# Optimization experiments

Hardware: AMD Instinct MI355X
Metric: run time of the kernel (lower is better)

The kernel has to match this reference:

```python
import jax, jax.numpy as jnp
import numpy as np

EPS = 1e-5
AVG_D = 32.0


def setup_inputs() -> dict:
    key = jax.random.key(0)
    ks = jax.random.split(key, 12)
    Ns, Nd, E, D, K = 1_000_000, 100_000, 3_200_000, 16, 2
    Fs, Fd, V = 4, 4, 100_000
    F = Fd + K  # predictor fields
    inp = {}
    inp["Cat_src"] = jax.random.randint(ks[0], (Ns, Fs), 0, V)
    inp["Cat_dst"] = jax.random.randint(ks[1], (Nd, Fd), 0, V)
    inp["src_ids"] = jax.random.randint(ks[2], (E,), 0, Ns)
    inp["dst_ids"] = jax.random.randint(ks[3], (E,), 0, Nd)
    inp["label"] = jax.random.randint(ks[4], (Nd,), 0, 2)
    inp["w"] = jax.random.normal(ks[5], (V, D), dtype=jnp.float32) * 0.05
    inp["W_agg"] = jax.random.normal(ks[6], (K, 12 * D, D), dtype=jnp.float32) * 0.05
    inp["b_agg"] = jnp.zeros((K, D), jnp.float32)
    inp["w_lin"] = jax.random.normal(ks[7], (F * D,), dtype=jnp.float32) * 0.05
    inp["b_lin"] = jnp.zeros((1,), jnp.float32)
    inp["W1"] = jax.random.normal(ks[8], (F * D, 64), dtype=jnp.float32) * 0.05
    inp["b1"] = jnp.zeros((64,), jnp.float32)
    inp["W2"] = jax.random.normal(ks[9], (64, 32), dtype=jnp.float32) * 0.05
    inp["b2"] = jnp.zeros((32,), jnp.float32)
    inp["W3"] = jax.random.normal(ks[10], (32, 1), dtype=jnp.float32) * 0.05
    inp["b3"] = jnp.zeros((1,), jnp.float32)
    return inp


def reference(Cat_src, Cat_dst, src_ids, dst_ids, label, w, W_agg, b_agg,
              w_lin, b_lin, W1, b1, W2, b2, W3, b3):
    Nd = Cat_dst.shape[0]
    # --- node embedding: gather cat fields, RowEmb with modes [mean, max] -> [Ns, K, D]
    emb = w[Cat_src]                                      # [Ns, Fs, D]
    h_src = jnp.stack([emb.mean(1), emb.max(1)], axis=1)  # [Ns, K, D]
    # --- multi-aggregator message passing (copy_u + segment min/max/mean, std via mean of h^2)
    m = h_src[src_ids]                                    # [E, K, D]
    deg = jax.ops.segment_sum(jnp.ones(src_ids.shape, m.dtype), dst_ids, Nd)
    safe = jnp.maximum(deg, 1.0)[:, None, None]
    mean = jax.ops.segment_sum(m, dst_ids, Nd) / safe
    mean2 = jax.ops.segment_sum(m * m, dst_ids, Nd) / safe
    has = (deg > 0)[:, None, None]
    mn = jnp.where(has, jax.ops.segment_min(m, dst_ids, Nd), 0.0)
    mx = jnp.where(has, jax.ops.segment_max(m, dst_ids, Nd), 0.0)
    std = jnp.sqrt(jax.nn.relu(mean2 - mean * mean) + EPS)
    tmp = jnp.concatenate([mean, mn, mx, std], axis=-1)   # [Nd, K, 4D]
    # --- PNA degree scalers: identity / amplification / attenuation
    logd = jnp.log(deg + 1.0)
    log_avg = jnp.log(AVG_D + 1.0)
    amp = (logd / log_avg)[:, None, None]
    att = jnp.where(logd > 0, log_avg / jnp.maximum(logd, EPS), 0.0)[:, None, None]
    scaled = jnp.concatenate([tmp, tmp * amp, tmp * att], axis=-1)  # [Nd, K, 12D]
    mes = jnp.einsum('nkf,kfd->nkd', scaled, W_agg) + b_agg          # [Nd, K, D]
    # --- final block: concat dst cat embeddings with aggregated messages
    x = jnp.concatenate([w[Cat_dst], mes], axis=1)        # [Nd, F, D]
    # --- DeepFM predictor: linear + FM pairwise + deep MLP
    flat = x.reshape(Nd, -1)
    lin = flat @ w_lin + b_lin[0]
    s = x.sum(1)
    fm = 0.5 * ((s * s) - (x * x).sum(1)).sum(-1)
    h = jax.nn.relu(flat @ W1 + b1)
    h = jax.nn.relu(h @ W2 + b2)
    deep = (h @ W3 + b3)[:, 0]
    pred = jax.nn.sigmoid(lin + fm + deep)
    return (pred, label)
```

## Files before the change

kernel.cpp:

```cpp
#include <hip/hip_runtime.h>
#include <math.h>

#define EPSF 1e-5f
#define BSH  5
#define BSZ  32
#define MAXB 4096
#define SBH  9
#define MAXSB 256
#define TILE 4096
#define SEG  8
#define BCAP 1472
#define XPAD 100
#define X2PADS 72
#define HISTB 512
#define NPACK 14336

typedef __attribute__((ext_vector_type(8))) short short8;
typedef __attribute__((ext_vector_type(4))) float float4v;

__device__ inline unsigned f2bf_rne(float x) {
    unsigned u = __float_as_uint(x);
    u += 0x7FFF + ((u >> 16) & 1);
    return u >> 16;
}
__device__ inline short bf16_of(float x) { return (short)f2bf_rne(x); }
__device__ inline float bf2f_lo(unsigned hv) { return __uint_as_float(hv << 16); }
__device__ inline float bf2f_hi(unsigned hv) { return __uint_as_float(hv & 0xFFFF0000u); }
__device__ inline float bf2f_s(ushort s) { return __uint_as_float((unsigned)s << 16); }

__global__ void cast_w(const float* __restrict__ w, ushort* __restrict__ wb, int n) {
    int i4 = (blockIdx.x * 256 + threadIdx.x) * 4;
    if (i4 + 3 < n) {
        float4 v = *(const float4*)(w + i4);
        ushort4 o;
        o.x = (ushort)f2bf_rne(v.x); o.y = (ushort)f2bf_rne(v.y);
        o.z = (ushort)f2bf_rne(v.z); o.w = (ushort)f2bf_rne(v.w);
        *(ushort4*)(wb + i4) = o;
    } else {
        for (int j = i4; j < n; ++j) wb[j] = (ushort)f2bf_rne(w[j]);
    }
}

__global__ __launch_bounds__(256) void zero_pack(
    int* bcount, int nb,
    const float* __restrict__ W_agg, const float* __restrict__ W1,
    const float* __restrict__ W2, ushort* __restrict__ wpack)
{
    int nzb = (nb + 255) >> 8;
    if ((int)blockIdx.x < nzb) {
        int i = blockIdx.x * 256 + threadIdx.x;
        if (i < nb) bcount[i] = 0;
        return;
    }
    for (int it = threadIdx.x; it < 1792; it += 256) {
        if (it < 768) {
            int t_g = it >> 6; int rem = it & 63;
            int q = rem >> 4, col = rem & 15;
            int kvar = t_g / 6, t = t_g % 6;
            const float* src = W_agg + kvar * 3072 + (t * 32 + q * 8) * 16 + col;
            ushort* dst = wpack + (size_t)it * 8;
#pragma unroll
            for (int j = 0; j < 8; ++j) dst[j] = (ushort)f2bf_rne(src[j * 16]);
        } else if (it < 1536) {
            int i2 = it - 768;
            int t = i2 >> 8; int rem = i2 & 255;
            int q = rem >> 6, col = rem & 63;
            const float* src = W1 + (t * 32 + q * 8) * 64 + col;
            ushort* dst = wpack + 6144 + (size_t)i2 * 8;
#pragma unroll
            for (int j = 0; j < 8; ++j) dst[j] = (ushort)f2bf_rne(src[j * 64]);
        } else {
            int i2 = it - 1536;
            int t = i2 >> 7; int rem = i2 & 127;
            int q = rem >> 5, col = rem & 31;
            const float* src = W2 + (t * 32 + q * 8) * 32 + col;
            ushort* dst = wpack + 12288 + (size_t)i2 * 8;
#pragma unroll
            for (int j = 0; j < 8; ++j) dst[j] = (ushort)f2bf_rne(src[j * 32]);
        }
    }
}

__global__ __launch_bounds__(256) void build_h_hist(
    const int* __restrict__ Cat_src, const ushort* __restrict__ wb,
    unsigned* __restrict__ h, int Ns,
    const int* __restrict__ dst_ids, int* bcount, int E, int nb)
{
    __shared__ int hsh[MAXB];
    if (blockIdx.x < HISTB) {
        for (int i = threadIdx.x; i < nb; i += 256) hsh[i] = 0;
        __syncthreads();
        int stride = HISTB * 256;
        for (int e = blockIdx.x * 256 + threadIdx.x; e < E; e += stride)
            atomicAdd(&hsh[dst_ids[e] >> BSH], 1);
        __syncthreads();
        for (int i = threadIdx.x; i < nb; i += 256) {
            int c = hsh[i];
            if (c) atomicAdd(&bcount[i], c);
        }
        return;
    }
    int gid = (blockIdx.x - HISTB) * 256 + threadIdx.x;
    int s = gid >> 4;
    if (s >= Ns) return;
    int lane = threadIdx.x & 63;
    int d = lane & 15;
    int c = Cat_src[s * 4 + (d & 3)];
    float vs = 0.f, vm = -INFINITY;
#pragma unroll
    for (int f = 0; f < 4; ++f) {
        int id = __shfl(c, (lane & 48) + f, 64);
        float a = bf2f_s(wb[id * 16 + d]);
        vs += a; vm = fmaxf(vm, a);
    }
    unsigned packed = f2bf_rne(vs * 0.25f) | (f2bf_rne(vm) << 16);
    __builtin_nontemporal_store(packed, &h[s * 16 + d]);
}

__global__ __launch_bounds__(256) void scan_buckets(const int* __restrict__ bcount,
                                                    int* bstart, int* sbcursor,
                                                    int* gcur, int nb) {
    __shared__ int lsum[256];
    int tid = threadIdx.x;
    int v[16];
    int s = 0;
#pragma unroll
    for (int j = 0; j < 16; ++j) {
        int idx = tid * 16 + j;
        v[j] = (idx < nb) ? bcount[idx] : 0;
        s += v[j];
    }
    lsum[tid] = s;
    __syncthreads();
    for (int off = 1; off < 256; off <<= 1) {
        int y = (tid >= off) ? lsum[tid - off] : 0;
        __syncthreads();
        lsum[tid] += y;
        __syncthreads();
    }
    int run = lsum[tid] - s;
    if (tid * 16 < nb) sbcursor[tid] = run;
#pragma unroll
    for (int j = 0; j < 16; ++j) {
        int idx = tid * 16 + j;
        if (idx < nb) { bstart[idx] = run; gcur[idx] = run; }
        run += v[j];
    }
}

__global__ __launch_bounds__(256) void scatter_sb(
    const int* __restrict__ src_ids, const int* __restrict__ dst_ids,
    int* sbcursor, unsigned* __restrict__ pairs1, int E, int nsb)
{
    __shared__ int cnt[MAXSB];
    __shared__ int base[MAXSB];
    int tid = threadIdx.x;
    int t0 = blockIdx.x * TILE;
    for (int i = tid; i < nsb; i += 256) cnt[i] = 0;
    __syncthreads();
    int rank[TILE / 256];
#pragma unroll
    for (int j = 0; j < TILE / 256; ++j) {
        int e = t0 + j * 256 + tid;
        rank[j] = (e < E) ? atomicAdd(&cnt[dst_ids[e] >> SBH], 1) : 0;
    }
    __syncthreads();
    for (int i = tid; i < nsb; i += 256) {
        int c = cnt[i];
        base[i] = c ? atomicAdd(&sbcursor[i], c) : 0;
    }
    __syncthreads();
#pragma unroll
    for (int j = 0; j < TILE / 256; ++j) {
        int e = t0 + j * 256 + tid;
        if (e < E) {
            int d = dst_ids[e];
            int sb = d >> SBH;
            pairs1[base[sb] + rank[j]] =
                ((unsigned)src_ids[e] << 9) | (unsigned)(d & 511);
        }
    }
}

__global__ __launch_bounds__(256) void scatter_fine(
    const unsigned* __restrict__ pairs1, const int* __restrict__ bstart,
    int* gcur, unsigned* __restrict__ pairs2, int nb, int nsb, int E)
{
    __shared__ int cnt[16];
    __shared__ int base[16];
    int S = blockIdx.x >> 3, seg = blockIdx.x & (SEG - 1);
    int tid = threadIdx.x;
    int sbs = bstart[S << 4];
    int sbe = (S == nsb - 1) ? E : bstart[(S + 1) << 4];
    int len = sbe - sbs;
    int per = (len + SEG - 1) / SEG;
    int s0 = sbs + seg * per;
    int s1 = s0 + per; if (s1 > sbe) s1 = sbe;
    if (tid < 16) cnt[tid] = 0;
    __syncthreads();
    int rank[12];
    unsigned pv[12];
    int nit = (s1 - s0 + 255) >> 8;
    if (nit > 12) nit = 12;
    for (int j = 0; j < nit; ++j) {
        int e = s0 + j * 256 + tid;
        if (e < s1) {
            unsigned p = __builtin_nontemporal_load(&pairs1[e]);
            pv[j] = p;
            rank[j] = atomicAdd(&cnt[(p >> 5) & 15], 1);
        }
    }
    __syncthreads();
    if (tid < 16) {
        int idx = (S << 4) + tid;
        int c = cnt[tid];
        base[tid] = (c && idx < nb) ? atomicAdd(&gcur[idx], c) : 0;
    }
    __syncthreads();
    for (int j = 0; j < nit; ++j) {
        int e = s0 + j * 256 + tid;
        if (e < s1) {
            unsigned p = pv[j];
            pairs2[base[(p >> 5) & 15] + rank[j]] = p;
        }
    }
}


__device__ inline void bucket_sort(const unsigned* __restrict__ pairs,
                                   int gbase, int cnt,
                                   unsigned* sp, int* hist, int* ofs, int* start,
                                   int tid)
{
    if (tid < BSZ) hist[tid] = 0;
    __syncthreads();
    for (int i = tid; i < cnt; i += 256)
        atomicAdd(&hist[__builtin_nontemporal_load(&pairs[gbase + i]) & (BSZ - 1)], 1);
    __syncthreads();
    if (tid < BSZ) ofs[tid] = hist[tid];
    __syncthreads();
    for (int off = 1; off < BSZ; off <<= 1) {
        int y = (tid < BSZ && tid >= off) ? ofs[tid - off] : 0;
        __syncthreads();
        if (tid < BSZ) ofs[tid] += y;
        __syncthreads();
    }
    if (tid < BSZ) {
        start[tid] = ofs[tid] - hist[tid];
        ofs[tid] = ofs[tid] - hist[tid];
    }
    __syncthreads();
    for (int i = tid; i < cnt; i += 256) {
        unsigned p = __builtin_nontemporal_load(&pairs[gbase + i]);
        int r = atomicAdd(&ofs[p & (BSZ - 1)], 1);
        sp[r] = p;
    }
    __syncthreads();
}

__device__ inline void emit_stats(float sum0, float sq0, float mn0, float mx0,
                                  float sum1, float sq1, float mn1, float mx1,
                                  int dg, int n, int lane, int sub,
                                  ushort* __restrict__ tmpb, int* __restrict__ deg_out)
{
#pragma unroll
    for (int off = 16; off <= 32; off <<= 1) {
        sum0 += __shfl_xor(sum0, off); sq0 += __shfl_xor(sq0, off);
        mn0 = fminf(mn0, __shfl_xor(mn0, off)); mx0 = fmaxf(mx0, __shfl_xor(mx0, off));
        sum1 += __shfl_xor(sum1, off); sq1 += __shfl_xor(sq1, off);
        mn1 = fminf(mn1, __shfl_xor(mn1, off)); mx1 = fmaxf(mx1, __shfl_xor(mx1, off));
    }
    float safe = fmaxf((float)dg, 1.f);
    float r = 1.f / safe;
    bool has = dg > 0;
    float mean0 = sum0 * r, mean1 = sum1 * r;
    float sd0 = sqrtf(fmaxf(sq0 * r - mean0 * mean0, 0.f) + EPSF);
    float sd1 = sqrtf(fmaxf(sq1 * r - mean1 * mean1, 0.f) + EPSF);
    float v0 = (sub == 0) ? mean0 : (sub == 1) ? (has ? mn0 : 0.f)
             : (sub == 2) ? (has ? mx0 : 0.f) : sd0;
    float v1 = (sub == 0) ? mean1 : (sub == 1) ? (has ? mn1 : 0.f)
             : (sub == 2) ? (has ? mx1 : 0.f) : sd1;
    ushort* tp = tmpb + (size_t)n * 128;
    tp[lane] = (ushort)f2bf_rne(v0);
    tp[64 + lane] = (ushort)f2bf_rne(v1);
    if (lane == 0) deg_out[n] = dg;
}

__global__ __launch_bounds__(256) void agg_from_h(
    const unsigned* __restrict__ h,
    const int* __restrict__ bstart, const int* __restrict__ bcount,
    const unsigned* __restrict__ pairs,
    ushort* __restrict__ tmpb, int* __restrict__ deg_out, int Nd)
{
    __shared__ unsigned sp[BCAP];
    __shared__ int hist[BSZ];
    __shared__ int ofs[BSZ];
    __shared__ int start[BSZ];
    int b = blockIdx.x, tid = threadIdx.x;
    int cnt = bcount[b];
    int gbase = bstart[b];
    if (cnt > BCAP) cnt = BCAP;
    bucket_sort(pairs, gbase, cnt, sp, hist, ofs, start, tid);

    int wv = tid >> 6, lane = tid & 63, sub = lane >> 4, d = lane & 15;
#pragma unroll 1
    for (int q = 0; q < 8; ++q) {
        int dl = wv * 8 + q;
        int n = b * BSZ + dl;
        if (n >= Nd) break;
        int st = start[dl], dg = hist[dl];
        float sum0 = 0.f, sq0 = 0.f, mn0 = INFINITY, mx0 = -INFINITY;
        float sum1 = 0.f, sq1 = 0.f, mn1 = INFINITY, mx1 = -INFINITY;
        int nt = (dg + 15) >> 4;
        for (int t = 0; t < nt; ++t) {
            int base = t * 16 + sub;
            unsigned hv[4];
#pragma unroll
            for (int j = 0; j < 4; ++j) {
                int e = base + j * 4;
                int ec = (e < dg) ? e : (dg - 1);
                unsigned p = sp[st + ec];
                hv[j] = h[(p >> 9) * 16 + d];
            }
#pragma unroll
            for (int j = 0; j < 4; ++j) {
                int e = base + j * 4;
                if (e < dg) {
                    float me = bf2f_lo(hv[j]);
                    float vm = bf2f_hi(hv[j]);
                    sum0 += me; sq0 += me * me;
                    mn0 = fminf(mn0, me); mx0 = fmaxf(mx0, me);
                    sum1 += vm; sq1 += vm * vm;
                    mn1 = fminf(mn1, vm); mx1 = fmaxf(mx1, vm);
                }
            }
        }
        emit_stats(sum0, sq0, mn0, mx0, sum1, sq1, mn1, mx1,
                   dg, n, lane, sub, tmpb, deg_out);
    }
}

__global__ __launch_bounds__(256) void agg_from_w(
    const int* __restrict__ Cat_src, const float* __restrict__ w,
    const ushort* __restrict__ wb, int use_bf,
    const int* __restrict__ bstart, const int* __restrict__ bcount,
    const unsigned* __restrict__ pairs,
    ushort* __restrict__ tmpb, int* __restrict__ deg_out, int Nd)
{
    __shared__ unsigned sp[BCAP];
    __shared__ int hist[BSZ];
    __shared__ int ofs[BSZ];
    __shared__ int start[BSZ];
    int b = blockIdx.x, tid = threadIdx.x;
    int cnt = bcount[b];
    int gbase = bstart[b];
    if (cnt > BCAP) cnt = BCAP;
    bucket_sort(pairs, gbase, cnt, sp, hist, ofs, start, tid);

    int wv = tid >> 6, lane = tid & 63, sub = lane >> 4, d = lane & 15;
#pragma unroll 1
    for (int q = 0; q < 8; ++q) {
        int dl = wv * 8 + q;
        int n = b * BSZ + dl;
        if (n >= Nd) break;
        int st = start[dl], dg = hist[dl];
        float sum0 = 0.f, sq0 = 0.f, mn0 = INFINITY, mx0 = -INFINITY;
        float sum1 = 0.f, sq1 = 0.f, mn1 = INFINITY, mx1 = -INFINITY;
        int nt = (dg + 3) >> 2;
        for (int t = 0; t < nt; ++t) {
            int e4 = t * 4 + sub;
            int ec = (e4 < dg) ? e4 : (dg - 1);
            unsigned p = sp[st + ec];
            int src = (int)(p >> 9);
            int cat = Cat_src[src * 4 + (d & 3)];
            float vs = 0.f, vm = -INFINITY;
            if (use_bf) {
#pragma unroll
                for (int f = 0; f < 4; ++f) {
                    int id = __shfl(cat, sub * 16 + f, 64);
                    float a = bf2f_s(wb[id * 16 + d]);
                    vs += a; vm = fmaxf(vm, a);
                }
            } else {
#pragma unroll
                for (int f = 0; f < 4; ++f) {
                    int id = __shfl(cat, sub * 16 + f, 64);
                    float a = w[id * 16 + d];
                    vs += a; vm = fmaxf(vm, a);
                }
            }
            if (e4 < dg) {
                float me = vs * 0.25f;
                sum0 += me; sq0 += me * me;
                mn0 = fminf(mn0, me); mx0 = fmaxf(mx0, me);
                sum1 += vm; sq1 += vm * vm;
                mn1 = fminf(mn1, vm); mx1 = fmaxf(mx1, vm);
            }
        }
        emit_stats(sum0, sq0, mn0, mx0, sum1, sq1, mn1, mx1,
                   dg, n, lane, sub, tmpb, deg_out);
    }
}

__global__ __launch_bounds__(256) void finalize_mfma(
    const int* __restrict__ Cat_dst, const int* __restrict__ label,
    const float* __restrict__ w, const ushort* __restrict__ wpack,
    const float* __restrict__ b_agg,
    const float* __restrict__ w_lin, const float* __restrict__ b_lin,
    const float* __restrict__ b1, const float* __restrict__ b2,
    const float* __restrict__ W3, const float* __restrict__ b3,
    const int* __restrict__ deg_arr, const ushort* __restrict__ tmpb,
    float* __restrict__ out, int Nd)
{
    __shared__ __align__(16) float sx[4][16 * XPAD];
    __shared__ __align__(16) ushort sx2[4][16 * X2PADS];
    __shared__ float sdeep[4][16];

    int tid = threadIdx.x;
    int wv = tid >> 6, lane = tid & 63;
    int q = lane >> 4, m = lane & 15;
    int n0 = (blockIdx.x * 4 + wv) * 16;
    int n = n0 + m;
    int nc = (n < Nd) ? n : (Nd - 1);

    float* X = sx[wv];
    ushort* X2 = sx2[wv];

    float fdeg = (float)deg_arr[nc];
    float logd = logf(fdeg + 1.f);
    const float logavg = logf(33.0f);
    float amp = logd / logavg;
    float att = (logd > 0.f) ? (logavg / fmaxf(logd, EPSF)) : 0.f;
    float ampr[4], attr[4];
#pragma unroll
    for (int r = 0; r < 4; ++r) {
        ampr[r] = __shfl(amp, q * 4 + r, 64);
        attr[r] = __shfl(att, q * 4 + r, 64);
    }

    const ushort* tpn = tmpb + (size_t)nc * 128;
#pragma unroll
    for (int kvar = 0; kvar < 2; ++kvar) {
        short8 af0 = *(const short8*)(tpn + kvar * 64 + q * 8);
        short8 af1 = *(const short8*)(tpn + kvar * 64 + 32 + q * 8);
        float4v aI = {0.f,0.f,0.f,0.f}, aA = {0.f,0.f,0.f,0.f}, aT = {0.f,0.f,0.f,0.f};
#pragma unroll
        for (int sb = 0; sb < 3; ++sb) {
            short8 b0 = *(const short8*)(wpack +
                (size_t)(((kvar * 6 + sb * 2) * 4 + q) * 16 + m) * 8);
            short8 b1v = *(const short8*)(wpack +
                (size_t)(((kvar * 6 + sb * 2 + 1) * 4 + q) * 16 + m) * 8);
            if (sb == 0) {
                aI = __builtin_amdgcn_mfma_f32_16x16x32_bf16(af0, b0, aI, 0, 0, 0);
                aI = __builtin_amdgcn_mfma_f32_16x16x32_bf16(af1, b1v, aI, 0, 0, 0);
            } else if (sb == 1) {
                aA = __builtin_amdgcn_mfma_f32_16x16x32_bf16(af0, b0, aA, 0, 0, 0);
                aA = __builtin_amdgcn_mfma_f32_16x16x32_bf16(af1, b1v, aA, 0, 0, 0);
            } else {
                aT = __builtin_amdgcn_mfma_f32_16x16x32_bf16(af0, b0, aT, 0, 0, 0);
                aT = __builtin_amdgcn_mfma_f32_16x16x32_bf16(af1, b1v, aT, 0, 0, 0);
            }
        }
        float bias = b_agg[kvar * 16 + m];
#pragma unroll
        for (int r = 0; r < 4; ++r)
            X[(q * 4 + r) * XPAD + 64 + kvar * 16 + m] =
                aI[r] + ampr[r] * aA[r] + attr[r] * aT[r] + bias;
    }
    {
        int nl = lane >> 2, fl = lane & 3;
        int nn = n0 + nl;
        int nnc = (nn < Nd) ? nn : (Nd - 1);
        int cid = Cat_dst[nnc * 4 + fl];
        const float4* R = (const float4*)(w + (size_t)cid * 16);
        float* xp = X + nl * XPAD + fl * 16;
        *(float4*)(xp + 0)  = R[0];
        *(float4*)(xp + 4)  = R[1];
        *(float4*)(xp + 8)  = R[2];
        *(float4*)(xp + 12) = R[3];
    }
    __syncthreads();

    float lin = 0.f, sq = 0.f;
    float sd[16];
#pragma unroll
    for (int u = 0; u < 16; ++u) sd[u] = 0.f;
    {
        const float* xp = X + m * XPAD + q * 16;
        const float* wl = w_lin + q * 16;
#pragma unroll
        for (int u = 0; u < 16; ++u) {
            float v = xp[u];
            lin += v * wl[u]; sq += v * v; sd[u] += v;
        }
    }
    if (q < 2) {
        const float* xp = X + m * XPAD + (4 + q) * 16;
        const float* wl = w_lin + (4 + q) * 16;
#pragma unroll
        for (int u = 0; u < 16; ++u) {
            float v = xp[u];
            lin += v * wl[u]; sq += v * v; sd[u] += v;
        }
    }
#pragma unroll
    for (int off = 16; off <= 32; off <<= 1) {
        lin += __shfl_xor(lin, off);
        sq  += __shfl_xor(sq, off);
#pragma unroll
        for (int u = 0; u < 16; ++u) sd[u] += __shfl_xor(sd[u], off);
    }
    float fm = 0.f;
#pragma unroll
    for (int u = 0; u < 16; ++u) fm += sd[u] * sd[u];
    fm = 0.5f * (fm - sq);

    short8 xa[3];
#pragma unroll
    for (int t = 0; t < 3; ++t) {
        const float* xp = X + m * XPAD + t * 32 + q * 8;
        float4 a0 = *(const float4*)xp;
        float4 a1 = *(const float4*)(xp + 4);
        xa[t][0] = bf16_of(a0.x); xa[t][1] = bf16_of(a0.y);
        xa[t][2] = bf16_of(a0.z); xa[t][3] = bf16_of(a0.w);
        xa[t][4] = bf16_of(a1.x); xa[t][5] = bf16_of(a1.y);
        xa[t][6] = bf16_of(a1.z); xa[t][7] = bf16_of(a1.w);
    }
#pragma unroll
    for (int nt = 0; nt < 4; ++nt) {
        float4v acc = {0.f, 0.f, 0.f, 0.f};
#pragma unroll
        for (int t = 0; t < 3; ++t) {
            short8 bf = *(const short8*)(wpack + 6144 +
                (size_t)((t * 4 + q) * 64 + nt * 16 + m) * 8);
            acc = __builtin_amdgcn_mfma_f32_16x16x32_bf16(xa[t], bf, acc, 0, 0, 0);
        }
        float bb = b1[nt * 16 + m];
#pragma unroll
        for (int r = 0; r < 4; ++r)
            X2[(q * 4 + r) * X2PADS + nt * 16 + m] =
                (ushort)f2bf_rne(fmaxf(acc[r] + bb, 0.f));
    }
    __syncthreads();

    short8 ha[2];
#pragma unroll
    for (int t = 0; t < 2; ++t)
        ha[t] = *(const short8*)(X2 + m * X2PADS + t * 32 + q * 8);
    float dp[4] = {0.f, 0.f, 0.f, 0.f};
#pragma unroll
    for (int nt = 0; nt < 2; ++nt) {
        float4v acc = {0.f, 0.f, 0.f, 0.f};
#pragma unroll
        for (int t = 0; t < 2; ++t) {
            short8 bf = *(const short8*)(wpack + 12288 +
                (size_t)((t * 4 + q) * 32 + nt * 16 + m) * 8);
            acc = __builtin_amdgcn_mfma_f32_16x16x32_bf16(ha[t], bf, acc, 0, 0, 0);
        }
        float bb = b2[nt * 16 + m];
        float w3 = W3[nt * 16 + m];
#pragma unroll
        for (int r = 0; r < 4; ++r)
            dp[r] += fmaxf(acc[r] + bb, 0.f) * w3;
    }
#pragma unroll
    for (int off = 1; off <= 8; off <<= 1) {
#pragma unroll
        for (int r = 0; r < 4; ++r) dp[r] += __shfl_xor(dp[r], off);
    }
    if (m < 4)
        sdeep[wv][q * 4 + m] = (m == 0) ? dp[0] : (m == 1) ? dp[1]
                             : (m == 2) ? dp[2] : dp[3];
    __syncthreads();
    float deep = sdeep[wv][m];

    if (q == 0 && n < Nd) {
        float z = lin + b_lin[0] + fm + deep + b3[0];
        float pred = 1.f / (1.f + expf(-z));
        out[n] = pred;
        out[Nd + n] = (float)label[n];
    }
}

extern "C" void kernel_launch(void* const* d_in, const int* in_sizes, int n_in,
                              void* d_out, int out_size, void* d_ws, size_t ws_size,
                              hipStream_t stream) {
    const int*   Cat_src = (const int*)d_in[0];
    const int*   Cat_dst = (const int*)d_in[1];
    const int*   src_ids = (const int*)d_in[2];
    const int*   dst_ids = (const int*)d_in[3];
    const int*   label   = (const int*)d_in[4];
    const float* w       = (const float*)d_in[5];
    const float* W_agg   = (const float*)d_in[6];
    const float* b_agg   = (const float*)d_in[7];
    const float* w_lin   = (const float*)d_in[8];
    const float* b_lin   = (const float*)d_in[9];
    const float* W1      = (const float*)d_in[10];
    const float* b1      = (const float*)d_in[11];
    const float* W2      = (const float*)d_in[12];
    const float* b2      = (const float*)d_in[13];
    const float* W3      = (const float*)d_in[14];
    const float* b3      = (const float*)d_in[15];

    int E  = in_sizes[2];
    int Nd = in_sizes[4];
    int Ns = in_sizes[0] / 4;
    int VD = in_sizes[5];
    int nb  = (Nd + BSZ - 1) >> BSH;
    int nsb = (nb + 15) >> 4;

    int* bcount   = (int*)d_ws;
    int* bstart   = bcount + MAXB;
    int* sbcursor = bstart + MAXB;
    int* gcur     = sbcursor + MAXSB;
    int* deg      = gcur + MAXB;
    unsigned* pairs1 = (unsigned*)(deg + Nd);
    unsigned* pairs2 = pairs1 + E;
    size_t off_tmp = (((size_t)(MAXB * 3 + MAXSB + Nd) + 2 * (size_t)E) * 4 + 255)
                     & ~(size_t)255;
    ushort* tmpb = (ushort*)((char*)d_ws + off_tmp);
    ushort* wpack = tmpb + (size_t)Nd * 128;
    ushort* w_bf16 = wpack + NPACK;
    unsigned* h  = (unsigned*)(w_bf16 + VD);

    size_t need_common = off_tmp + (size_t)Nd * 256 + (size_t)NPACK * 2;
    size_t need_A = need_common + (size_t)VD * 2;
    size_t need_B = need_A + (size_t)Ns * 64;
    int mode = (ws_size >= need_B) ? 2 : (ws_size >= need_A) ? 1 : 0;

    float* out = (float*)d_out;

    int nzb = (nb + 255) >> 8;
    hipLaunchKernelGGL(zero_pack, dim3(nzb + 1), dim3(256), 0, stream,
                       bcount, nb, W_agg, W1, W2, wpack);
    if (mode >= 1)
        hipLaunchKernelGGL(cast_w, dim3((VD / 4 + 255) / 256), dim3(256),
                           0, stream, w, w_bf16, VD);
    if (mode == 2) {
        int hb = (int)(((size_t)Ns * 16 + 255) / 256);
        hipLaunchKernelGGL(build_h_hist, dim3(HISTB + hb), dim3(256), 0, stream,
                           Cat_src, w_bf16, h, Ns, dst_ids, bcount, E, nb);
    } else {
        hipLaunchKernelGGL(build_h_hist, dim3(HISTB), dim3(256), 0, stream,
                           Cat_src, w_bf16, h, 0, dst_ids, bcount, E, nb);
    }
    hipLaunchKernelGGL(scan_buckets, dim3(1), dim3(256), 0, stream,
                       bcount, bstart, sbcursor, gcur, nb);
    hipLaunchKernelGGL(scatter_sb, dim3((E + TILE - 1) / TILE), dim3(256), 0, stream,
                       src_ids, dst_ids, sbcursor, pairs1, E, nsb);
    hipLaunchKernelGGL(scatter_fine, dim3(nsb * SEG), dim3(256), 0, stream,
                       pairs1, bstart, gcur, pairs2, nb, nsb, E);
    if (mode == 2) {
        hipLaunchKernelGGL(agg_from_h, dim3(nb), dim3(256), 0, stream,
                           h, bstart, bcount, pairs2, tmpb, deg, Nd);
    } else {
        hipLaunchKernelGGL(agg_from_w, dim3(nb), dim3(256), 0, stream,
                           Cat_src, w, w_bf16, mode, bstart, bcount, pairs2,
                           tmpb, deg, Nd);
    }
    hipLaunchKernelGGL(finalize_mfma, dim3((Nd + 63) / 64), dim3(256), 0, stream,
                       Cat_dst, label, w, wpack, b_agg, w_lin, b_lin,
                       b1, b2, W3, b3, deg, tmpb, out, Nd);
}
```

Measured before the change: 322.0 us.

## Regroup setup kernels, co-schedule h build with scatter, widen gather unroll, bf16 X tile

Merges zero_pack and cast_w into one setup kernel. The h-embedding build moves out of the histogram kernel and runs as extra blocks alongside the super-bucket scatter. The per-destination gather loop now issues eight h loads per iteration instead of four, for more memory-level parallelism. The finalize kernel's X tile is stored in shared memory as bf16, which halves its LDS footprint and removes the per-use float-to-bf16 conversion before the MFMA. In exchange, the linear and FM terms now read bf16-rounded inputs, and register pressure in the aggregation loop rises.

```diff
diff --git a/kernel.cpp b/kernel.cpp
--- a/kernel.cpp
+++ b/kernel.cpp
@@ -10,7 +10,7 @@
 #define TILE 4096
 #define SEG  8
 #define BCAP 1472
-#define XPAD 100
+#define XPADS2 104
 #define X2PADS 72
 #define HISTB 512
 #define NPACK 14336
@@ -28,93 +28,75 @@
 __device__ inline float bf2f_hi(unsigned hv) { return __uint_as_float(hv & 0xFFFF0000u); }
 __device__ inline float bf2f_s(ushort s) { return __uint_as_float((unsigned)s << 16); }
 
-__global__ void cast_w(const float* __restrict__ w, ushort* __restrict__ wb, int n) {
-    int i4 = (blockIdx.x * 256 + threadIdx.x) * 4;
-    if (i4 + 3 < n) {
+__global__ __launch_bounds__(256) void setup_all(
+    int* bcount, int nb,
+    const float* __restrict__ W_agg, const float* __restrict__ W1,
+    const float* __restrict__ W2, ushort* __restrict__ wpack,
+    const float* __restrict__ w, ushort* __restrict__ wb, int VD, int do_cast)
+{
+    int nzb = (nb + 255) >> 8;
+    int bid = blockIdx.x;
+    if (bid < nzb) {
+        int i = bid * 256 + threadIdx.x;
+        if (i < nb) bcount[i] = 0;
+        return;
+    }
+    if (bid == nzb) {
+        for (int it = threadIdx.x; it < 1792; it += 256) {
+            if (it < 768) {
+                int t_g = it >> 6; int rem = it & 63;
+                int q = rem >> 4, col = rem & 15;
+                int kvar = t_g / 6, t = t_g % 6;
+                const float* src = W_agg + kvar * 3072 + (t * 32 + q * 8) * 16 + col;
+                ushort* dst = wpack + (size_t)it * 8;
+#pragma unroll
+                for (int j = 0; j < 8; ++j) dst[j] = (ushort)f2bf_rne(src[j * 16]);
+            } else if (it < 1536) {
+                int i2 = it - 768;
+                int t = i2 >> 8; int rem = i2 & 255;
+                int q = rem >> 6, col = rem & 63;
+                const float* src = W1 + (t * 32 + q * 8) * 64 + col;
+                ushort* dst = wpack + 6144 + (size_t)i2 * 8;
+#pragma unroll
+                for (int j = 0; j < 8; ++j) dst[j] = (ushort)f2bf_rne(src[j * 64]);
+            } else {
+                int i2 = it - 1536;
+                int t = i2 >> 7; int rem = i2 & 127;
+                int q = rem >> 5, col = rem & 31;
+                const float* src = W2 + (t * 32 + q * 8) * 32 + col;
+                ushort* dst = wpack + 12288 + (size_t)i2 * 8;
+#pragma unroll
+                for (int j = 0; j < 8; ++j) dst[j] = (ushort)f2bf_rne(src[j * 32]);
+            }
+        }
+        return;
+    }
+    if (!do_cast) return;
+    int i4 = ((bid - nzb - 1) * 256 + threadIdx.x) * 4;
+    if (i4 + 3 < VD) {
         float4 v = *(const float4*)(w + i4);
         ushort4 o;
         o.x = (ushort)f2bf_rne(v.x); o.y = (ushort)f2bf_rne(v.y);
         o.z = (ushort)f2bf_rne(v.z); o.w = (ushort)f2bf_rne(v.w);
         *(ushort4*)(wb + i4) = o;
     } else {
-        for (int j = i4; j < n; ++j) wb[j] = (ushort)f2bf_rne(w[j]);
-    }
-}
-
-__global__ __launch_bounds__(256) void zero_pack(
-    int* bcount, int nb,
-    const float* __restrict__ W_agg, const float* __restrict__ W1,
-    const float* __restrict__ W2, ushort* __restrict__ wpack)
-{
-    int nzb = (nb + 255) >> 8;
-    if ((int)blockIdx.x < nzb) {
-        int i = blockIdx.x * 256 + threadIdx.x;
-        if (i < nb) bcount[i] = 0;
-        return;
-    }
-    for (int it = threadIdx.x; it < 1792; it += 256) {
-        if (it < 768) {
-            int t_g = it >> 6; int rem = it & 63;
-            int q = rem >> 4, col = rem & 15;
-            int kvar = t_g / 6, t = t_g % 6;
-            const float* src = W_agg + kvar * 3072 + (t * 32 + q * 8) * 16 + col;
-            ushort* dst = wpack + (size_t)it * 8;
-#pragma unroll
-            for (int j = 0; j < 8; ++j) dst[j] = (ushort)f2bf_rne(src[j * 16]);
-        } else if (it < 1536) {
-            int i2 = it - 768;
-            int t = i2 >> 8; int rem = i2 & 255;
-            int q = rem >> 6, col = rem & 63;
-            const float* src = W1 + (t * 32 + q * 8) * 64 + col;
-            ushort* dst = wpack + 6144 + (size_t)i2 * 8;
-#pragma unroll
-            for (int j = 0; j < 8; ++j) dst[j] = (ushort)f2bf_rne(src[j * 64]);
-        } else {
-            int i2 = it - 1536;
-            int t = i2 >> 7; int rem = i2 & 127;
-            int q = rem >> 5, col = rem & 31;
-            const float* src = W2 + (t * 32 + q * 8) * 32 + col;
-            ushort* dst = wpack + 12288 + (size_t)i2 * 8;
-#pragma unroll
-            for (int j = 0; j < 8; ++j) dst[j] = (ushort)f2bf_rne(src[j * 32]);
-        }
-    }
-}
-
-__global__ __launch_bounds__(256) void build_h_hist(
-    const int* __restrict__ Cat_src, const ushort* __restrict__ wb,
-    unsigned* __restrict__ h, int Ns,
-    const int* __restrict__ dst_ids, int* bcount, int E, int nb)
-{
+        for (int j = i4; j < VD; ++j) wb[j] = (ushort)f2bf_rne(w[j]);
+    }
+}
+
+__global__ __launch_bounds__(256) void hist_fine(const int* __restrict__ dst_ids,
+                                                 int* bcount, int E, int nb) {
     __shared__ int hsh[MAXB];
-    if (blockIdx.x < HISTB) {
-        for (int i = threadIdx.x; i < nb; i += 256) hsh[i] = 0;
-        __syncthreads();
-        int stride = HISTB * 256;
-        for (int e = blockIdx.x * 256 + threadIdx.x; e < E; e += stride)
-            atomicAdd(&hsh[dst_ids[e] >> BSH], 1);
-        __syncthreads();
-        for (int i = threadIdx.x; i < nb; i += 256) {
-            int c = hsh[i];
-            if (c) atomicAdd(&bcount[i], c);
-        }
-        return;
-    }
-    int gid = (blockIdx.x - HISTB) * 256 + threadIdx.x;
-    int s = gid >> 4;
-    if (s >= Ns) return;
-    int lane = threadIdx.x & 63;
-    int d = lane & 15;
-    int c = Cat_src[s * 4 + (d & 3)];
-    float vs = 0.f, vm = -INFINITY;
-#pragma unroll
-    for (int f = 0; f < 4; ++f) {
-        int id = __shfl(c, (lane & 48) + f, 64);
-        float a = bf2f_s(wb[id * 16 + d]);
-        vs += a; vm = fmaxf(vm, a);
-    }
-    unsigned packed = f2bf_rne(vs * 0.25f) | (f2bf_rne(vm) << 16);
-    __builtin_nontemporal_store(packed, &h[s * 16 + d]);
+    for (int i = threadIdx.x; i < nb; i += 256) hsh[i] = 0;
+    __syncthreads();
+    int stride = HISTB * 256;
+    for (int e = blockIdx.x * 256 + threadIdx.x; e < E; e += stride)
+        atomicAdd(&hsh[dst_ids[e] >> BSH], 1);
+    __syncthreads();
+    for (int i = threadIdx.x; i < nb; i += 256) {
+        int c = hsh[i];
+        if (c) atomicAdd(&bcount[i], c);
+    }
 }
 
 __global__ __launch_bounds__(256) void scan_buckets(const int* __restrict__ bcount,
@@ -148,13 +130,33 @@
     }
 }
 
-__global__ __launch_bounds__(256) void scatter_sb(
+__global__ __launch_bounds__(256) void sb_build(
     const int* __restrict__ src_ids, const int* __restrict__ dst_ids,
-    int* sbcursor, unsigned* __restrict__ pairs1, int E, int nsb)
+    int* sbcursor, unsigned* __restrict__ pairs1, int E, int nsb, int nst,
+    const int* __restrict__ Cat_src, const ushort* __restrict__ wb,
+    unsigned* __restrict__ h, int Ns)
 {
     __shared__ int cnt[MAXSB];
     __shared__ int base[MAXSB];
     int tid = threadIdx.x;
+    if ((int)blockIdx.x >= nst) {
+        long long gid = (long long)(blockIdx.x - nst) * 256 + tid;
+        int s = (int)(gid >> 4);
+        if (s >= Ns) return;
+        int lane = tid & 63;
+        int d = lane & 15;
+        int c = Cat_src[s * 4 + (d & 3)];
+        float vs = 0.f, vm = -INFINITY;
+#pragma unroll
+        for (int f = 0; f < 4; ++f) {
+            int id = __shfl(c, (lane & 48) + f, 64);
+            float a = bf2f_s(wb[id * 16 + d]);
+            vs += a; vm = fmaxf(vm, a);
+        }
+        unsigned packed = f2bf_rne(vs * 0.25f) | (f2bf_rne(vm) << 16);
+        __builtin_nontemporal_store(packed, &h[s * 16 + d]);
+        return;
+    }
     int t0 = blockIdx.x * TILE;
     for (int i = tid; i < nsb; i += 256) cnt[i] = 0;
     __syncthreads();
@@ -311,19 +313,19 @@
         int st = start[dl], dg = hist[dl];
         float sum0 = 0.f, sq0 = 0.f, mn0 = INFINITY, mx0 = -INFINITY;
         float sum1 = 0.f, sq1 = 0.f, mn1 = INFINITY, mx1 = -INFINITY;
-        int nt = (dg + 15) >> 4;
+        int nt = (dg + 31) >> 5;
         for (int t = 0; t < nt; ++t) {
-            int base = t * 16 + sub;
-            unsigned hv[4];
-#pragma unroll
-            for (int j = 0; j < 4; ++j) {
+            int base = t * 32 + sub;
+            unsigned hv[8];
+#pragma unroll
+            for (int j = 0; j < 8; ++j) {
                 int e = base + j * 4;
                 int ec = (e < dg) ? e : (dg - 1);
                 unsigned p = sp[st + ec];
                 hv[j] = h[(p >> 9) * 16 + d];
             }
 #pragma unroll
-            for (int j = 0; j < 4; ++j) {
+            for (int j = 0; j < 8; ++j) {
                 int e = base + j * 4;
                 if (e < dg) {
                     float me = bf2f_lo(hv[j]);
@@ -412,7 +414,7 @@
     const int* __restrict__ deg_arr, const ushort* __restrict__ tmpb,
     float* __restrict__ out, int Nd)
 {
-    __shared__ __align__(16) float sx[4][16 * XPAD];
+    __shared__ __align__(16) ushort sx[4][16 * XPADS2];
     __shared__ __align__(16) ushort sx2[4][16 * X2PADS];
     __shared__ float sdeep[4][16];
 
@@ -423,7 +425,7 @@
     int n = n0 + m;
     int nc = (n < Nd) ? n : (Nd - 1);
 
-    float* X = sx[wv];
+    ushort* X = sx[wv];
     ushort* X2 = sx2[wv];
 
     float fdeg = (float)deg_arr[nc];
@@ -464,8 +466,8 @@
         float bias = b_agg[kvar * 16 + m];
 #pragma unroll
         for (int r = 0; r < 4; ++r)
-            X[(q * 4 + r) * XPAD + 64 + kvar * 16 + m] =
-                aI[r] + ampr[r] * aA[r] + attr[r] * aT[r] + bias;
+            X[(q * 4 + r) * XPADS2 + 64 + kvar * 16 + m] = (ushort)f2bf_rne(
+                aI[r] + ampr[r] * aA[r] + attr[r] * aT[r] + bias);
     }
     {
         int nl = lane >> 2, fl = lane & 3;
@@ -473,11 +475,19 @@
         int nnc = (nn < Nd) ? nn : (Nd - 1);
         int cid = Cat_dst[nnc * 4 + fl];
         const float4* R = (const float4*)(w + (size_t)cid * 16);
-        float* xp = X + nl * XPAD + fl * 16;
-        *(float4*)(xp + 0)  = R[0];
-        *(float4*)(xp + 4)  = R[1];
-        *(float4*)(xp + 8)  = R[2];
-        *(float4*)(xp + 12) = R[3];
+        float4 r0 = R[0], r1 = R[1], r2 = R[2], r3 = R[3];
+        short8 o0, o1;
+        o0[0] = bf16_of(r0.x); o0[1] = bf16_of(r0.y);
+        o0[2] = bf16_of(r0.z); o0[3] = bf16_of(r0.w);
+        o0[4] = bf16_of(r1.x); o0[5] = bf16_of(r1.y);
+        o0[6] = bf16_of(r1.z); o0[7] = bf16_of(r1.w);
+        o1[0] = bf16_of(r2.x); o1[1] = bf16_of(r2.y);
+        o1[2] = bf16_of(r2.z); o1[3] = bf16_of(r2.w);
+        o1[4] = bf16_of(r3.x); o1[5] = bf16_of(r3.y);
+        o1[6] = bf16_of(r3.z); o1[7] = bf16_of(r3.w);
+        ushort* xp = X + nl * XPADS2 + fl * 16;
+        *(short8*)(xp) = o0;
+        *(short8*)(xp + 8) = o1;
     }
     __syncthreads();
 
@@ -486,20 +496,20 @@
 #pragma unroll
     for (int u = 0; u < 16; ++u) sd[u] = 0.f;
     {
-        const float* xp = X + m * XPAD + q * 16;
+        const ushort* xp = X + m * XPADS2 + q * 16;
         const float* wl = w_lin + q * 16;
 #pragma unroll
         for (int u = 0; u < 16; ++u) {
-            float v = xp[u];
+            float v = bf2f_s(xp[u]);
             lin += v * wl[u]; sq += v * v; sd[u] += v;
         }
     }
     if (q < 2) {
-        const float* xp = X + m * XPAD + (4 + q) * 16;
+        const ushort* xp = X + m * XPADS2 + (4 + q) * 16;
         const float* wl = w_lin + (4 + q) * 16;
 #pragma unroll
         for (int u = 0; u < 16; ++u) {
-            float v = xp[u];
+            float v = bf2f_s(xp[u]);
             lin += v * wl[u]; sq += v * v; sd[u] += v;
         }
     }
@@ -517,15 +527,8 @@
 
     short8 xa[3];
 #pragma unroll
-    for (int t = 0; t < 3; ++t) {
-        const float* xp = X + m * XPAD + t * 32 + q * 8;
-        float4 a0 = *(const float4*)xp;
-        float4 a1 = *(const float4*)(xp + 4);
-        xa[t][0] = bf16_of(a0.x); xa[t][1] = bf16_of(a0.y);
-        xa[t][2] = bf16_of(a0.z); xa[t][3] = bf16_of(a0.w);
-        xa[t][4] = bf16_of(a1.x); xa[t][5] = bf16_of(a1.y);
-        xa[t][6] = bf16_of(a1.z); xa[t][7] = bf16_of(a1.w);
-    }
+    for (int t = 0; t < 3; ++t)
+        xa[t] = *(const short8*)(X + m * XPADS2 + t * 32 + q * 8);
 #pragma unroll
     for (int nt = 0; nt < 4; ++nt) {
         float4v acc = {0.f, 0.f, 0.f, 0.f};
@@ -608,6 +611,7 @@
     int VD = in_sizes[5];
     int nb  = (Nd + BSZ - 1) >> BSH;
     int nsb = (nb + 15) >> 4;
+    int nst = (E + TILE - 1) / TILE;
 
     int* bcount   = (int*)d_ws;
     int* bstart   = bcount + MAXB;
@@ -631,23 +635,19 @@
     float* out = (float*)d_out;
 
     int nzb = (nb + 255) >> 8;
-    hipLaunchKernelGGL(zero_pack, dim3(nzb + 1), dim3(256), 0, stream,
-                       bcount, nb, W_agg, W1, W2, wpack);
-    if (mode >= 1)
-        hipLaunchKernelGGL(cast_w, dim3((VD / 4 + 255) / 256), dim3(256),
-                           0, stream, w, w_bf16, VD);
-    if (mode == 2) {
-        int hb = (int)(((size_t)Ns * 16 + 255) / 256);
-        hipLaunchKernelGGL(build_h_hist, dim3(HISTB + hb), dim3(256), 0, stream,
-                           Cat_src, w_bf16, h, Ns, dst_ids, bcount, E, nb);
-    } else {
-        hipLaunchKernelGGL(build_h_hist, dim3(HISTB), dim3(256), 0, stream,
-                           Cat_src, w_bf16, h, 0, dst_ids, bcount, E, nb);
-    }
+    int ncb = (mode >= 1) ? (VD / 4 + 255) / 256 : 0;
+    hipLaunchKernelGGL(setup_all, dim3(nzb + 1 + ncb), dim3(256), 0, stream,
+                       bcount, nb, W_agg, W1, W2, wpack, w, w_bf16, VD, mode >= 1);
+    hipLaunchKernelGGL(hist_fine, dim3(HISTB), dim3(256), 0, stream,
+                       dst_ids, bcount, E, nb);
     hipLaunchKernelGGL(scan_buckets, dim3(1), dim3(256), 0, stream,
                        bcount, bstart, sbcursor, gcur, nb);
-    hipLaunchKernelGGL(scatter_sb, dim3((E + TILE - 1) / TILE), dim3(256), 0, stream,
-                       src_ids, dst_ids, sbcursor, pairs1, E, nsb);
+    {
+        int hb = (mode == 2) ? (int)(((size_t)Ns * 16 + 255) / 256) : 0;
+        hipLaunchKernelGGL(sb_build, dim3(nst + hb), dim3(256), 0, stream,
+                           src_ids, dst_ids, sbcursor, pairs1, E, nsb, nst,
+                           Cat_src, w_bf16, h, (mode == 2) ? Ns : 0);
+    }
     hipLaunchKernelGGL(scatter_fine, dim3(nsb * SEG), dim3(256), 0, stream,
                        pairs1, bstart, gcur, pairs2, nb, nsb, E);
     if (mode == 2) {
```

After: 337.5 us. 4.8% more time.
